# Kernel optimization log

Measured on AMD Instinct MI355X. Metric: run time of the kernel, lower is better.

Reference implementation:

```python
import jax, jax.numpy as jnp
import numpy as np

SHIFT = 1  # fixed shift_direction for determinism


def setup_inputs() -> dict:
    key = jax.random.key(0)
    k1, k2, k3 = jax.random.split(key, 3)
    x = jax.random.normal(k1, (1, 256, 28, 28), dtype=jnp.float32)
    w1 = jax.random.normal(k2, (8, 64, 3), dtype=jnp.float32)
    w2 = jax.random.normal(k3, (32, 4, 3), dtype=jnp.float32)
    return {"x": x, "w1": w1, "w2": w2}


def reference(x, w1, w2):
    # x: (1, 256, 28, 28) -> (64, 4, 28, 28); roll along H (axis 2 here == torch axis 3)
    t = x.reshape(64, 4, 28, 28)
    t = jnp.roll(t, SHIFT, axis=2)
    # unfold over H, kernel 3, pad 1: tap j at output row m reads padded row m+j
    p = jnp.pad(t, ((0, 0), (0, 0), (1, 1), (0, 0)))
    taps = jnp.stack([p[:, :, j:j + 28, :] for j in range(3)], axis=2)  # (64,4,3,28,28)
    # grouped conv over H: mix 64 input channels -> 8 output channels, per group o=4
    t4 = jnp.einsum('iojmn,kij->komn', taps, w1)  # (8,4,28,28)
    # unfold over W, kernel 3, pad 1
    p2 = jnp.pad(t4, ((0, 0), (0, 0), (0, 0), (1, 1)))
    taps2 = jnp.stack([p2[:, :, :, k:k + 28] for k in range(3)], axis=3)  # (8,4,28,3,28)
    # grouped conv over W: mix 4 groups -> 32 channels, per group o=8
    t6 = jnp.einsum('ojmkn,ijk->iomn', taps2, w2)  # (32,8,28,28)
    return t6.reshape(1, 256, 28, 28)
```

## Files before the change

kernel.cpp:

```cpp
#include <hip/hip_runtime.h>

__global__ __launch_bounds__(256) void fused_shiftconv(const float* __restrict__ x,
                                                       const float* __restrict__ w1,
                                                       const float* __restrict__ w2,
                                                       float* __restrict__ out) {
    __shared__ float w1s[8 * 193];
    __shared__ float w2s[384];
    __shared__ float t4s[32 * 33];

    const int tid = threadIdx.x;
    const int m = blockIdx.x;

    for (int idx = tid; idx < 1536; idx += 256) {
        const int k = idx / 192;
        w1s[k * 193 + (idx - k * 192)] = w1[idx];
    }
    if (tid < 128) {
        w2s[tid] = w2[tid];
        w2s[tid + 128] = w2[tid + 128];
        w2s[tid + 256] = w2[tid + 256];
    }
    if (tid < 64) {
        t4s[(tid & 31) * 33 + (tid >> 5) * 29] = 0.f;
    }
    __syncthreads();

    if (tid < 224) {
        const int o = tid / 56;
        const int q = (tid >> 3) % 7;
        const int k = tid & 7;
        const float* wk = &w1s[k * 193];
        float4 acc = make_float4(0.f, 0.f, 0.f, 0.f);
#pragma unroll
        for (int j = 0; j < 3; ++j) {
            const int mj = m + j;
            if (mj == 0 || mj == 29) continue;
            int hh = mj - 2;
            if (hh < 0) hh += 28;
            const float* xb = x + o * 784 + hh * 28 + q * 4;
#pragma unroll 8
            for (int i = 0; i < 64; ++i) {
                const float4 v = *reinterpret_cast<const float4*>(xb + i * 3136);
                const float w = wk[i * 3 + j];
                acc.x = fmaf(w, v.x, acc.x);
                acc.y = fmaf(w, v.y, acc.y);
                acc.z = fmaf(w, v.z, acc.z);
                acc.w = fmaf(w, v.w, acc.w);
            }
        }
        float* dst = &t4s[(k * 4 + o) * 33 + 1 + q * 4];
        dst[0] = acc.x; dst[1] = acc.y; dst[2] = acc.z; dst[3] = acc.w;
    }
    __syncthreads();

    const int i2 = tid >> 3;
    const int o2 = tid & 7;
    const float* wr = &w2s[i2 * 12];
    float* orow = out + (i2 * 8 + o2) * 784 + m * 28;
#pragma unroll
    for (int q = 0; q < 7; ++q) {
        float4 r;
        float* rp = &r.x;
#pragma unroll
        for (int e = 0; e < 4; ++e) {
            const int n = q * 4 + e;
            float acc = 0.f;
#pragma unroll
            for (int j = 0; j < 4; ++j) {
                const float* trow = &t4s[(o2 * 4 + j) * 33 + n];
#pragma unroll
                for (int kk = 0; kk < 3; ++kk) {
                    acc = fmaf(wr[j * 3 + kk], trow[kk], acc);
                }
            }
            rp[e] = acc;
        }
        *reinterpret_cast<float4*>(orow + q * 4) = r;
    }
}

extern "C" void kernel_launch(void* const* d_in, const int* in_sizes, int n_in,
                              void* d_out, int out_size, void* d_ws, size_t ws_size,
                              hipStream_t stream) {
    const float* x  = (const float*)d_in[0];
    const float* w1 = (const float*)d_in[1];
    const float* w2 = (const float*)d_in[2];
    float* out = (float*)d_out;

    fused_shiftconv<<<dim3(28), 256, 0, stream>>>(x, w1, w2, out);
}
```

Before: 72.69 us.

## Split work across output-channel blocks to launch 224 blocks instead of 28

The grid grows from one block per output row to one block per (row, k-channel) pair, giving 224 blocks that spread over more compute units. Each block computes only its slice of the first-stage conv (112 threads, scalar loads) and then the second stage with one float4 output per thread. Weights for stage one are read directly from global memory rather than staged in shared memory. The trade-off is that input x is re-read by 8 blocks per row and each thread loses its float4 vector loads.

```diff
diff --git a/kernel.cpp b/kernel.cpp
--- a/kernel.cpp
+++ b/kernel.cpp
@@ -1,82 +1,59 @@
 #include <hip/hip_runtime.h>
 
-__global__ __launch_bounds__(256) void fused_shiftconv(const float* __restrict__ x,
+__global__ __launch_bounds__(224) void fused_shiftconv(const float* __restrict__ x,
                                                        const float* __restrict__ w1,
                                                        const float* __restrict__ w2,
                                                        float* __restrict__ out) {
-    __shared__ float w1s[8 * 193];
     __shared__ float w2s[384];
-    __shared__ float t4s[32 * 33];
+    __shared__ float t4s[4][32];
 
     const int tid = threadIdx.x;
-    const int m = blockIdx.x;
+    const int m  = blockIdx.x >> 3;
+    const int o2 = blockIdx.x & 7;
 
-    for (int idx = tid; idx < 1536; idx += 256) {
-        const int k = idx / 192;
-        w1s[k * 193 + (idx - k * 192)] = w1[idx];
-    }
-    if (tid < 128) {
-        w2s[tid] = w2[tid];
-        w2s[tid + 128] = w2[tid + 128];
-        w2s[tid + 256] = w2[tid + 256];
-    }
-    if (tid < 64) {
-        t4s[(tid & 31) * 33 + (tid >> 5) * 29] = 0.f;
-    }
-    __syncthreads();
+    for (int idx = tid; idx < 384; idx += 224) w2s[idx] = w2[idx];
+    if (tid < 8) t4s[tid >> 1][(tid & 1) * 29] = 0.f;
 
-    if (tid < 224) {
-        const int o = tid / 56;
-        const int q = (tid >> 3) % 7;
-        const int k = tid & 7;
-        const float* wk = &w1s[k * 193];
-        float4 acc = make_float4(0.f, 0.f, 0.f, 0.f);
+    if (tid < 112) {
+        const int o = tid / 28;
+        const int n = tid - o * 28;
+        const float* wp = w1 + o2 * 192;
+        float acc = 0.f;
 #pragma unroll
         for (int j = 0; j < 3; ++j) {
             const int mj = m + j;
             if (mj == 0 || mj == 29) continue;
             int hh = mj - 2;
             if (hh < 0) hh += 28;
-            const float* xb = x + o * 784 + hh * 28 + q * 4;
-#pragma unroll 8
+            const float* xp = x + o * 784 + hh * 28 + n;
+#pragma unroll
             for (int i = 0; i < 64; ++i) {
-                const float4 v = *reinterpret_cast<const float4*>(xb + i * 3136);
-                const float w = wk[i * 3 + j];
-                acc.x = fmaf(w, v.x, acc.x);
-                acc.y = fmaf(w, v.y, acc.y);
-                acc.z = fmaf(w, v.z, acc.z);
-                acc.w = fmaf(w, v.w, acc.w);
+                acc = fmaf(wp[i * 3 + j], xp[i * 3136], acc);
             }
         }
-        float* dst = &t4s[(k * 4 + o) * 33 + 1 + q * 4];
-        dst[0] = acc.x; dst[1] = acc.y; dst[2] = acc.z; dst[3] = acc.w;
+        t4s[o][n + 1] = acc;
     }
     __syncthreads();
 
-    const int i2 = tid >> 3;
-    const int o2 = tid & 7;
+    const int i2 = tid / 7;
+    const int q  = tid - i2 * 7;
     const float* wr = &w2s[i2 * 12];
-    float* orow = out + (i2 * 8 + o2) * 784 + m * 28;
+    float4 r;
+    float* rp = &r.x;
 #pragma unroll
-    for (int q = 0; q < 7; ++q) {
-        float4 r;
-        float* rp = &r.x;
+    for (int e = 0; e < 4; ++e) {
+        const int n = q * 4 + e;
+        float acc = 0.f;
 #pragma unroll
-        for (int e = 0; e < 4; ++e) {
-            const int n = q * 4 + e;
-            float acc = 0.f;
+        for (int j = 0; j < 4; ++j) {
 #pragma unroll
-            for (int j = 0; j < 4; ++j) {
-                const float* trow = &t4s[(o2 * 4 + j) * 33 + n];
-#pragma unroll
-                for (int kk = 0; kk < 3; ++kk) {
-                    acc = fmaf(wr[j * 3 + kk], trow[kk], acc);
-                }
+            for (int kk = 0; kk < 3; ++kk) {
+                acc = fmaf(wr[j * 3 + kk], t4s[j][n + kk], acc);
             }
-            rp[e] = acc;
         }
-        *reinterpret_cast<float4*>(orow + q * 4) = r;
+        rp[e] = acc;
     }
+    *reinterpret_cast<float4*>(out + (i2 * 8 + o2) * 784 + m * 28 + q * 4) = r;
 }
 
 extern "C" void kernel_launch(void* const* d_in, const int* in_sizes, int n_in,
@@ -87,5 +64,5 @@
     const float* w2 = (const float*)d_in[2];
     float* out = (float*)d_out;
 
-    fused_shiftconv<<<dim3(28), 256, 0, stream>>>(x, w1, w2, out);
+    fused_shiftconv<<<dim3(224), 224, 0, stream>>>(x, w1, w2, out);
 }
```

Measured after the change: 61.74 us. -15.1%, faster.
